# Kernel optimization log

Hardware: AMD Instinct MI355X
Metric: run time of the kernel (lower is better)

## Reference

```python
import jax, jax.numpy as jnp
import numpy as np

PI = 3.141592653589793


def setup_inputs() -> dict:
    key = jax.random.key(0)
    k1, k2, k3 = jax.random.split(key, 3)
    num_ent, num_rel2, emb_dim, batch = 50000, 50000, 256, 64
    # xavier_normal-ish init (std based on fan_in+fan_out)
    std_e = (2.0 / (num_ent + emb_dim)) ** 0.5
    std_r = (2.0 / (num_rel2 + emb_dim)) ** 0.5
    ent_emb = jax.random.normal(k1, (num_ent, emb_dim), dtype=jnp.float32) * std_e
    rel_emb = jax.random.normal(k2, (num_rel2, emb_dim), dtype=jnp.float32) * std_r
    triples = jax.random.randint(k3, (batch, 3), 0, num_ent, dtype=jnp.int64)
    return {"triples": triples, "ent_emb": ent_emb, "rel_emb": rel_emb}


def reference(triples, ent_emb, rel_emb):
    # Scalars computed from the tables at init time (.item() in torch -> constants)
    max_ent = jax.lax.stop_gradient(jnp.max(jnp.abs(ent_emb)))
    max_rel = jax.lax.stop_gradient(jnp.max(jnp.abs(rel_emb)))
    head = ent_emb[triples[:, 0]]            # [B, D]
    rel = rel_emb[triples[:, 1]]             # [B, D]
    phase_head = head / (max_ent / PI)       # [B, D]
    phase_rel = rel / (max_rel / PI)         # [B, D]
    phase_ent = ent_emb / (max_ent / PI)     # [N, D]
    # broadcast [B,1,D] - [1,N,D] -> [B,N,D], sin, sum over D -> [B,N]
    score = phase_head[:, None, :] + phase_rel[:, None, :] - phase_ent[None, :, :]
    return -jnp.sum(jnp.sin(score), axis=2)
```

## Files before the change

### kernel.cpp

```cpp
#include <hip/hip_runtime.h>
#include <hip/hip_bf16.h>


typedef __bf16 bf16x8 __attribute__((ext_vector_type(8)));
typedef float f32x4 __attribute__((ext_vector_type(4)));

#define EMB_D 256
#define KDIM 512
#define BATCH 64
#define NB_HALF 1024


__global__ __launch_bounds__(256) void absmax_stage1(
    const float* __restrict__ ent, const float* __restrict__ rel,
    int n_ent, int n_rel, float* __restrict__ partial) {
  const bool is_ent = (int)blockIdx.x < NB_HALF;
  const float* __restrict__ src = is_ent ? ent : rel;
  const int n = is_ent ? n_ent : n_rel;
  const int bid = is_ent ? (int)blockIdx.x : (int)blockIdx.x - NB_HALF;
  const int nvec = n >> 2;
  const float4* __restrict__ v = (const float4*)src;
  float m = 0.0f;
  for (int i = bid * 256 + threadIdx.x; i < nvec; i += NB_HALF * 256) {
    float4 x = v[i];
    m = fmaxf(m, fmaxf(fmaxf(fabsf(x.x), fabsf(x.y)),
                       fmaxf(fabsf(x.z), fabsf(x.w))));
  }
#pragma unroll
  for (int off = 32; off > 0; off >>= 1)
    m = fmaxf(m, __shfl_down(m, off, 64));
  __shared__ float sm[4];
  if ((threadIdx.x & 63) == 0) sm[threadIdx.x >> 6] = m;
  __syncthreads();
  if (threadIdx.x == 0)
    partial[blockIdx.x] = fmaxf(fmaxf(sm[0], sm[1]), fmaxf(sm[2], sm[3]));
}

__global__ __launch_bounds__(256) void absmax_stage2(
    const float* __restrict__ partial, float* __restrict__ wsf) {
  const int t = threadIdx.x;
  float me = 0.0f, mr = 0.0f;
#pragma unroll
  for (int i = 0; i < NB_HALF / 256; ++i) {
    me = fmaxf(me, partial[i * 256 + t]);
    mr = fmaxf(mr, partial[NB_HALF + i * 256 + t]);
  }
#pragma unroll
  for (int off = 32; off > 0; off >>= 1) {
    me = fmaxf(me, __shfl_down(me, off, 64));
    mr = fmaxf(mr, __shfl_down(mr, off, 64));
  }
  __shared__ float sme[4], smr[4];
  if ((t & 63) == 0) {
    sme[t >> 6] = me;
    smr[t >> 6] = mr;
  }
  __syncthreads();
  if (t == 0) {
    wsf[0] = fmaxf(fmaxf(sme[0], sme[1]), fmaxf(sme[2], sme[3]));
    wsf[1] = fmaxf(fmaxf(smr[0], smr[1]), fmaxf(smr[2], smr[3]));
  }
}

__global__ __launch_bounds__(256) void build_A_kernel(
    const int* __restrict__ triples, const float* __restrict__ ent,
    const float* __restrict__ rel, const float* __restrict__ wsf,
    unsigned int* __restrict__ A) {
  const int b = blockIdx.x;
  const int d = threadIdx.x;
  const float max_e = wsf[0];
  const float max_r = wsf[1];
  const int h = triples[b * 3 + 0];
  const int r = triples[b * 3 + 1];
  const float rev = ent[h * EMB_D + d] * (0.5f / max_e) +
                    rel[r * EMB_D + d] * (0.5f / max_r);
  const float s = __builtin_amdgcn_sinf(rev);
  const float c = __builtin_amdgcn_cosf(rev);
  const unsigned int cb = (unsigned int)__bfloat16_as_ushort(__float2bfloat16(c));
  const unsigned int nsb = (unsigned int)__bfloat16_as_ushort(__float2bfloat16(-s));
  A[b * (KDIM / 2) + d] = cb | (nsb << 16);
}

__global__ __launch_bounds__(64, 3) void score_kernel(
    const float* __restrict__ ent, const unsigned int* __restrict__ A,
    const float* __restrict__ wsf, float* __restrict__ out, int NE) {
  const int lane = threadIdx.x;
  const int lo = lane & 15;
  const int hi = lane >> 4;
  const int e = blockIdx.x * 16 + lo;
  const float scale = 0.5f / wsf[0];

  f32x4 acc[4];
#pragma unroll
  for (int mt = 0; mt < 4; ++mt)
#pragma unroll
    for (int r = 0; r < 4; ++r) acc[mt][r] = 0.0f;

  const float4* __restrict__ erow = (const float4*)(ent + (long)e * EMB_D);
  const uint4* __restrict__ A4 = (const uint4*)A;

  union UA {
    uint4 u;
    bf16x8 v;
  };

  float4 pe[16];
#pragma unroll
  for (int ks = 0; ks < 16; ++ks) pe[ks] = erow[ks * 4 + hi];

  uint4 a[3][4];
#pragma unroll
  for (int p = 0; p < 2; ++p)
#pragma unroll
    for (int mt = 0; mt < 4; ++mt)
      a[p][mt] = A4[(mt * 16 + lo) * 64 + p * 4 + hi];

#pragma unroll
  for (int ks = 0; ks < 16; ++ks) {
    if (ks + 2 < 16) {
#pragma unroll
      for (int mt = 0; mt < 4; ++mt)
        a[(ks + 2) % 3][mt] = A4[(mt * 16 + lo) * 64 + (ks + 2) * 4 + hi];
    }

    const float f0 = pe[ks].x * scale, f1 = pe[ks].y * scale,
                f2 = pe[ks].z * scale, f3 = pe[ks].w * scale;
    const float s0 = __builtin_amdgcn_sinf(f0), c0 = __builtin_amdgcn_cosf(f0);
    const float s1 = __builtin_amdgcn_sinf(f1), c1 = __builtin_amdgcn_cosf(f1);
    const float s2 = __builtin_amdgcn_sinf(f2), c2 = __builtin_amdgcn_cosf(f2);
    const float s3 = __builtin_amdgcn_sinf(f3), c3 = __builtin_amdgcn_cosf(f3);
    UA ub;
    ub.u.x = (unsigned int)__bfloat16_as_ushort(__float2bfloat16(s0)) |
             ((unsigned int)__bfloat16_as_ushort(__float2bfloat16(c0)) << 16);
    ub.u.y = (unsigned int)__bfloat16_as_ushort(__float2bfloat16(s1)) |
             ((unsigned int)__bfloat16_as_ushort(__float2bfloat16(c1)) << 16);
    ub.u.z = (unsigned int)__bfloat16_as_ushort(__float2bfloat16(s2)) |
             ((unsigned int)__bfloat16_as_ushort(__float2bfloat16(c2)) << 16);
    ub.u.w = (unsigned int)__bfloat16_as_ushort(__float2bfloat16(s3)) |
             ((unsigned int)__bfloat16_as_ushort(__float2bfloat16(c3)) << 16);

#pragma unroll
    for (int mt = 0; mt < 4; ++mt) {
      UA ua;
      ua.u = a[ks % 3][mt];
      acc[mt] = __builtin_amdgcn_mfma_f32_16x16x32_bf16(ua.v, ub.v, acc[mt], 0, 0, 0);
    }
  }

#pragma unroll
  for (int mt = 0; mt < 4; ++mt)
#pragma unroll
    for (int r = 0; r < 4; ++r)
      out[(long)(mt * 16 + hi * 4 + r) * NE + e] = acc[mt][r];
}

extern "C" void kernel_launch(void* const* d_in, const int* in_sizes, int n_in,
                              void* d_out, int out_size, void* d_ws,
                              size_t ws_size, hipStream_t stream) {
  const int* triples = (const int*)d_in[0];
  const float* ent = (const float*)d_in[1];
  const float* rel = (const float*)d_in[2];
  float* out = (float*)d_out;

  const int n_ent = in_sizes[1];
  const int n_rel = in_sizes[2];
  const int NE = n_ent / EMB_D;

  float* wsf = (float*)d_ws;
  float* partial = (float*)((char*)d_ws + 64);
  unsigned int* A = (unsigned int*)((char*)d_ws + 16384);

  absmax_stage1<<<2 * NB_HALF, 256, 0, stream>>>(ent, rel, n_ent, n_rel, partial);
  absmax_stage2<<<1, 256, 0, stream>>>(partial, wsf);
  build_A_kernel<<<BATCH, EMB_D, 0, stream>>>(triples, ent, rel, wsf, A);
  score_kernel<<<NE / 16, 64, 0, stream>>>(ent, A, wsf, out, NE);
}
```

Baseline: 57.18 us.

## Fuse absmax final reduction into build_A and restructure score kernel prefetch

Merges the second absmax reduction stage into the build_A kernel, so each of the 64 blocks redundantly reduces the partial maxima itself and one kernel launch plus a serial dependency disappears. The score kernel replaces the upfront load of all 16 entity float4s with a double-buffered prefetch of 4 at a time, deepens the A-operand prefetch from 2 to 3 steps, and drops the min-blocks launch bound. This is meant to cut register pressure and launch overhead, at the cost of redundant partial-max reads across blocks and possibly different occupancy or latency hiding.

```diff
diff --git a/kernel.cpp b/kernel.cpp
--- a/kernel.cpp
+++ b/kernel.cpp
@@ -21,6 +21,7 @@
   const int nvec = n >> 2;
   const float4* __restrict__ v = (const float4*)src;
   float m = 0.0f;
+#pragma unroll 2
   for (int i = bid * 256 + threadIdx.x; i < nvec; i += NB_HALF * 256) {
     float4 x = v[i];
     m = fmaxf(m, fmaxf(fmaxf(fabsf(x.x), fabsf(x.y)),
@@ -36,8 +37,10 @@
     partial[blockIdx.x] = fmaxf(fmaxf(sm[0], sm[1]), fmaxf(sm[2], sm[3]));
 }
 
-__global__ __launch_bounds__(256) void absmax_stage2(
-    const float* __restrict__ partial, float* __restrict__ wsf) {
+__global__ __launch_bounds__(256) void build_A_kernel(
+    const int* __restrict__ triples, const float* __restrict__ ent,
+    const float* __restrict__ rel, const float* __restrict__ partial,
+    float* __restrict__ wsf, unsigned int* __restrict__ A) {
   const int t = threadIdx.x;
   float me = 0.0f, mr = 0.0f;
 #pragma unroll
@@ -56,32 +59,25 @@
     smr[t >> 6] = mr;
   }
   __syncthreads();
-  if (t == 0) {
-    wsf[0] = fmaxf(fmaxf(sme[0], sme[1]), fmaxf(sme[2], sme[3]));
-    wsf[1] = fmaxf(fmaxf(smr[0], smr[1]), fmaxf(smr[2], smr[3]));
+  const float max_e = fmaxf(fmaxf(sme[0], sme[1]), fmaxf(sme[2], sme[3]));
+  const float max_r = fmaxf(fmaxf(smr[0], smr[1]), fmaxf(smr[2], smr[3]));
+  const int b = blockIdx.x;
+  if (b == 0 && t == 0) {
+    wsf[0] = max_e;
+    wsf[1] = max_r;
   }
-}
-
-__global__ __launch_bounds__(256) void build_A_kernel(
-    const int* __restrict__ triples, const float* __restrict__ ent,
-    const float* __restrict__ rel, const float* __restrict__ wsf,
-    unsigned int* __restrict__ A) {
-  const int b = blockIdx.x;
-  const int d = threadIdx.x;
-  const float max_e = wsf[0];
-  const float max_r = wsf[1];
   const int h = triples[b * 3 + 0];
   const int r = triples[b * 3 + 1];
-  const float rev = ent[h * EMB_D + d] * (0.5f / max_e) +
-                    rel[r * EMB_D + d] * (0.5f / max_r);
+  const float rev = ent[h * EMB_D + t] * (0.5f / max_e) +
+                    rel[r * EMB_D + t] * (0.5f / max_r);
   const float s = __builtin_amdgcn_sinf(rev);
   const float c = __builtin_amdgcn_cosf(rev);
   const unsigned int cb = (unsigned int)__bfloat16_as_ushort(__float2bfloat16(c));
   const unsigned int nsb = (unsigned int)__bfloat16_as_ushort(__float2bfloat16(-s));
-  A[b * (KDIM / 2) + d] = cb | (nsb << 16);
+  A[b * (KDIM / 2) + t] = cb | (nsb << 16);
 }
 
-__global__ __launch_bounds__(64, 3) void score_kernel(
+__global__ __launch_bounds__(64) void score_kernel(
     const float* __restrict__ ent, const unsigned int* __restrict__ A,
     const float* __restrict__ wsf, float* __restrict__ out, int NE) {
   const int lane = threadIdx.x;
@@ -104,27 +100,34 @@
     bf16x8 v;
   };
 
-  float4 pe[16];
+  float4 pq[2][4];
+  uint4 a[4][4];
+
 #pragma unroll
-  for (int ks = 0; ks < 16; ++ks) pe[ks] = erow[ks * 4 + hi];
-
-  uint4 a[3][4];
+  for (int j = 0; j < 4; ++j) pq[0][j] = erow[j * 4 + hi];
 #pragma unroll
-  for (int p = 0; p < 2; ++p)
+  for (int p = 0; p < 3; ++p)
 #pragma unroll
     for (int mt = 0; mt < 4; ++mt)
       a[p][mt] = A4[(mt * 16 + lo) * 64 + p * 4 + hi];
 
 #pragma unroll
   for (int ks = 0; ks < 16; ++ks) {
-    if (ks + 2 < 16) {
+    const int qsel = (ks >> 2) & 1;
+    if ((ks & 3) == 0 && ks + 4 < 16) {
+#pragma unroll
+      for (int j = 0; j < 4; ++j)
+        pq[qsel ^ 1][j] = erow[(ks + 4 + j) * 4 + hi];
+    }
+    if (ks + 3 < 16) {
 #pragma unroll
       for (int mt = 0; mt < 4; ++mt)
-        a[(ks + 2) % 3][mt] = A4[(mt * 16 + lo) * 64 + (ks + 2) * 4 + hi];
+        a[(ks + 3) & 3][mt] = A4[(mt * 16 + lo) * 64 + (ks + 3) * 4 + hi];
     }
 
-    const float f0 = pe[ks].x * scale, f1 = pe[ks].y * scale,
-                f2 = pe[ks].z * scale, f3 = pe[ks].w * scale;
+    const float4 pe = pq[qsel][ks & 3];
+    const float f0 = pe.x * scale, f1 = pe.y * scale, f2 = pe.z * scale,
+                f3 = pe.w * scale;
     const float s0 = __builtin_amdgcn_sinf(f0), c0 = __builtin_amdgcn_cosf(f0);
     const float s1 = __builtin_amdgcn_sinf(f1), c1 = __builtin_amdgcn_cosf(f1);
     const float s2 = __builtin_amdgcn_sinf(f2), c2 = __builtin_amdgcn_cosf(f2);
@@ -142,7 +145,7 @@
 #pragma unroll
     for (int mt = 0; mt < 4; ++mt) {
       UA ua;
-      ua.u = a[ks % 3][mt];
+      ua.u = a[ks & 3][mt];
       acc[mt] = __builtin_amdgcn_mfma_f32_16x16x32_bf16(ua.v, ub.v, acc[mt], 0, 0, 0);
     }
   }
@@ -171,7 +174,6 @@
   unsigned int* A = (unsigned int*)((char*)d_ws + 16384);
 
   absmax_stage1<<<2 * NB_HALF, 256, 0, stream>>>(ent, rel, n_ent, n_rel, partial);
-  absmax_stage2<<<1, 256, 0, stream>>>(partial, wsf);
-  build_A_kernel<<<BATCH, EMB_D, 0, stream>>>(triples, ent, rel, wsf, A);
+  build_A_kernel<<<BATCH, EMB_D, 0, stream>>>(triples, ent, rel, partial, wsf, A);
   score_kernel<<<NE / 16, 64, 0, stream>>>(ent, A, wsf, out, NE);
 }
```

New measurement: 56.24 us. About the same (-1.7%).
